# Kernel tuning notes

Hardware: AMD Instinct MI355X
Metric: run time of the kernel (lower is better)

Reference implementation:

```python
import jax, jax.numpy as jnp
import numpy as np

B, T, NN, H = 16, 64, 4096, 1024  # batch, seq_len, num_nodes**2, gru hidden


def _gru_layer(x, w_ih, w_hh, b_ih, b_hh):
    """PyTorch-semantics GRU layer, batch_first. x: [B, T, in] -> [B, T, H]."""
    h_dim = w_hh.shape[1]
    # precompute all input-side gate projections in one GEMM: [B, T, 3H]
    gates_x = jnp.einsum('bti,gi->btg', x, w_ih) + b_ih

    def step(h, gx):
        gh = h @ w_hh.T + b_hh                      # [B, 3H]
        xr, xz, xn = jnp.split(gx, 3, axis=-1)
        hr, hz, hn = jnp.split(gh, 3, axis=-1)
        r = jax.nn.sigmoid(xr + hr)
        z = jax.nn.sigmoid(xz + hz)
        n = jnp.tanh(xn + r * hn)
        h_new = (1.0 - z) * n + z * h
        return h_new, h_new

    h0 = jnp.zeros((x.shape[0], h_dim), x.dtype)
    _, ys = jax.lax.scan(step, h0, jnp.swapaxes(gates_x, 0, 1))  # time-major scan
    return jnp.swapaxes(ys, 0, 1)


def setup_inputs() -> dict:
    key = jax.random.key(0)
    ks = jax.random.split(key, 12)
    s_in, s_h = 1.0 / np.sqrt(NN), 1.0 / np.sqrt(H)
    return {
        'x':       jax.random.normal(ks[0], (B, T, NN), jnp.float32),
        'w_ih_l0': jax.random.normal(ks[1], (3 * H, NN), jnp.float32) * s_in,
        'w_hh_l0': jax.random.normal(ks[2], (3 * H, H), jnp.float32) * s_h,
        'b_ih_l0': jax.random.normal(ks[3], (3 * H,), jnp.float32) * s_h,
        'b_hh_l0': jax.random.normal(ks[4], (3 * H,), jnp.float32) * s_h,
        'w_ih_l1': jax.random.normal(ks[5], (3 * H, H), jnp.float32) * s_h,
        'w_hh_l1': jax.random.normal(ks[6], (3 * H, H), jnp.float32) * s_h,
        'b_ih_l1': jax.random.normal(ks[7], (3 * H,), jnp.float32) * s_h,
        'b_hh_l1': jax.random.normal(ks[8], (3 * H,), jnp.float32) * s_h,
        'dec_w':   jax.random.normal(ks[9], (NN, H), jnp.float32) * s_h,
        'dec_b':   jax.random.normal(ks[10], (NN,), jnp.float32) * s_h,
    }


def reference(x, w_ih_l0, w_hh_l0, b_ih_l0, b_hh_l0,
              w_ih_l1, w_hh_l1, b_ih_l1, b_hh_l1, dec_w, dec_b):
    # 2-layer GRU encode (batch_first), no dropout (eval / drop_p=0)
    h1 = _gru_layer(x, w_ih_l0, w_hh_l0, b_ih_l0, b_hh_l0)
    h2 = _gru_layer(h1, w_ih_l1, w_hh_l1, b_ih_l1, b_hh_l1)
    last = h2[:, -1, :]                               # [B, H] last timestep
    # per-sample decoder loop in the original == one batched GEMM here
    pred_graph_adj = last @ dec_w.T + dec_b           # [B, num_nodes**2]
    return pred_graph_adj
```

## Files before the change

### kernel.cpp

```cpp
#include <hip/hip_runtime.h>
#include <math.h>

constexpr int kB = 16;
constexpr int kT = 64;
constexpr int kH = 1024;

typedef short bf16x8 __attribute__((ext_vector_type(8)));
typedef float floatx4 __attribute__((ext_vector_type(4)));

__device__ __forceinline__ unsigned short f2bf_rne(float f) {
    unsigned u = __float_as_uint(f);
    u = u + 0x7FFFu + ((u >> 16) & 1u);
    return (unsigned short)(u >> 16);
}
__device__ __forceinline__ unsigned f2bf_fast_u(float f) {
    return (__float_as_uint(f) + 0x8000u) >> 16;
}
__device__ __forceinline__ uint4 pack8(const float4 a, const float4 b) {
    uint4 r;
    r.x = f2bf_fast_u(a.x) | (f2bf_fast_u(a.y) << 16);
    r.y = f2bf_fast_u(a.z) | (f2bf_fast_u(a.w) << 16);
    r.z = f2bf_fast_u(b.x) | (f2bf_fast_u(b.y) << 16);
    r.w = f2bf_fast_u(b.z) | (f2bf_fast_u(b.w) << 16);
    return r;
}

__device__ __forceinline__ void store_short_sys(unsigned short* p, unsigned v) {
    asm volatile("global_store_short %0, %1, off sc0 sc1"
                 :: "v"(p), "v"(v) : "memory");
}
__device__ __forceinline__ void store_dword_sys(unsigned* p, unsigned v) {
    asm volatile("global_store_dword %0, %1, off sc0 sc1"
                 :: "v"(p), "v"(v) : "memory");
}
__device__ __forceinline__ unsigned load_dword_sys(const unsigned* p) {
    unsigned v;
    asm volatile("global_load_dword %0, %1, off sc0 sc1\n\t"
                 "s_waitcnt vmcnt(0)"
                 : "=v"(v) : "v"(p) : "memory");
    return v;
}

__global__ __launch_bounds__(256)
void pack_bf16(const float* __restrict__ src, unsigned short* __restrict__ dst,
               int n4)
{
    const int i = blockIdx.x * 256 + threadIdx.x;
    if (i < n4) {
        const float4 v = ((const float4*)src)[i];
        ushort4 o;
        o.x = f2bf_rne(v.x); o.y = f2bf_rne(v.y);
        o.z = f2bf_rne(v.z); o.w = f2bf_rne(v.w);
        ((ushort4*)dst)[i] = o;
    }
}

#define GBM 64
#define GBN 64
#define GBK 16
#define GPAD 4

__global__ __launch_bounds__(256)
void gemm_nt_bias(const float* __restrict__ X, const float* __restrict__ W,
                  const float* __restrict__ bias, float* __restrict__ C,
                  int M, int N, int K)
{
    __shared__ float Xs[GBK][GBM + GPAD];
    __shared__ float Ws[GBK][GBN + GPAD];

    const int tid = threadIdx.x;
    const int bm = blockIdx.y * GBM;
    const int bn = blockIdx.x * GBN;
    const int tm = (tid >> 4) * 4;
    const int tn = (tid & 15) * 4;
    const int lr = tid >> 2;
    const int lc = (tid & 3) * 4;

    float acc[4][4] = {};

    for (int k0 = 0; k0 < K; k0 += GBK) {
        {
            const int gr = bm + lr;
            float4 v = make_float4(0.f, 0.f, 0.f, 0.f);
            if (gr < M) v = *(const float4*)(X + (long)gr * K + k0 + lc);
            Xs[lc + 0][lr] = v.x; Xs[lc + 1][lr] = v.y;
            Xs[lc + 2][lr] = v.z; Xs[lc + 3][lr] = v.w;
        }
        {
            const int gr = bn + lr;
            const float4 v = *(const float4*)(W + (long)gr * K + k0 + lc);
            Ws[lc + 0][lr] = v.x; Ws[lc + 1][lr] = v.y;
            Ws[lc + 2][lr] = v.z; Ws[lc + 3][lr] = v.w;
        }
        __syncthreads();
        #pragma unroll
        for (int k = 0; k < GBK; ++k) {
            const float4 a4 = *(const float4*)&Xs[k][tm];
            const float4 b4 = *(const float4*)&Ws[k][tn];
            acc[0][0] += a4.x * b4.x; acc[0][1] += a4.x * b4.y; acc[0][2] += a4.x * b4.z; acc[0][3] += a4.x * b4.w;
            acc[1][0] += a4.y * b4.x; acc[1][1] += a4.y * b4.y; acc[1][2] += a4.y * b4.z; acc[1][3] += a4.y * b4.w;
            acc[2][0] += a4.z * b4.x; acc[2][1] += a4.z * b4.y; acc[2][2] += a4.z * b4.z; acc[2][3] += a4.z * b4.w;
            acc[3][0] += a4.w * b4.x; acc[3][1] += a4.w * b4.y; acc[3][2] += a4.w * b4.z; acc[3][3] += a4.w * b4.w;
        }
        __syncthreads();
    }

    #pragma unroll
    for (int i = 0; i < 4; ++i) {
        const int gr = bm + tm + i;
        if (gr >= M) continue;
        #pragma unroll
        for (int jj = 0; jj < 4; ++jj) {
            const int gc = bn + tn + jj;
            C[(long)gr * N + gc] = acc[i][jj] + bias[gc];
        }
    }
}

__global__ __launch_bounds__(256)
void gemm_mfma_a(const float* __restrict__ X,
                 const float* __restrict__ W,
                 const float* __restrict__ bias,
                 float* __restrict__ C,
                 int M, int N, int K)
{
    __shared__ __attribute__((aligned(16))) unsigned short As[64 * 40];
    __shared__ __attribute__((aligned(16))) unsigned short Bs[128 * 40];

    const int tid  = threadIdx.x;
    const int lane = tid & 63;
    const int w    = tid >> 6;
    const int qm   = w & 1;
    const int qn   = w >> 1;
    const int bm   = blockIdx.y * 64;
    const int bn   = blockIdx.x * 128;
    const int al   = lane & 15;
    const int aq   = lane >> 4;

    floatx4 acc[2][4];
    #pragma unroll
    for (int i = 0; i < 2; ++i)
        #pragma unroll
        for (int j = 0; j < 4; ++j)
            acc[i][j] = (floatx4){0.f, 0.f, 0.f, 0.f};

    const int ar = tid >> 2;
    const int ak = (tid & 3) * 8;

    for (int k0 = 0; k0 < K; k0 += 32) {
        const float* ap = X + (long)(bm + ar) * K + k0 + ak;
        const float4 av0 = *(const float4*)(ap);
        const float4 av1 = *(const float4*)(ap + 4);
        float4 bv0[2], bv1[2];
        #pragma unroll
        for (int l = 0; l < 2; ++l) {
            const int c = tid + 256 * l;
            const float* bp = W + (long)(bn + (c >> 2)) * K + k0 + (c & 3) * 8;
            bv0[l] = *(const float4*)(bp);
            bv1[l] = *(const float4*)(bp + 4);
        }
        __syncthreads();
        *(uint4*)&As[ar * 40 + ak] = pack8(av0, av1);
        #pragma unroll
        for (int l = 0; l < 2; ++l) {
            const int c = tid + 256 * l;
            *(uint4*)&Bs[(c >> 2) * 40 + (c & 3) * 8] = pack8(bv0[l], bv1[l]);
        }
        __syncthreads();

        bf16x8 a[2], b[4];
        #pragma unroll
        for (int i = 0; i < 2; ++i)
            a[i] = *(const bf16x8*)&As[(qm * 32 + i * 16 + al) * 40 + aq * 8];
        #pragma unroll
        for (int j = 0; j < 4; ++j)
            b[j] = *(const bf16x8*)&Bs[(qn * 64 + j * 16 + al) * 40 + aq * 8];
        #pragma unroll
        for (int i = 0; i < 2; ++i)
            #pragma unroll
            for (int j = 0; j < 4; ++j)
                acc[i][j] = __builtin_amdgcn_mfma_f32_16x16x32_bf16(
                    a[i], b[j], acc[i][j], 0, 0, 0);
    }

    #pragma unroll
    for (int i = 0; i < 2; ++i) {
        #pragma unroll
        for (int j = 0; j < 4; ++j) {
            const int row0 = bm + qm * 32 + i * 16 + aq * 4;
            const int col  = bn + qn * 64 + j * 16 + al;
            const float bv = bias[col];
            #pragma unroll
            for (int r = 0; r < 4; ++r)
                C[(long)(row0 + r) * N + col] = acc[i][j][r] + bv;
        }
    }
}

#define FLAG_STRIDE 4

__global__ __launch_bounds__(768, 3)
void fused_gru_persistent(const float* __restrict__ gx0,
                          const unsigned short* __restrict__ w0, const float* __restrict__ bb0,
                          const unsigned short* __restrict__ w1, const float* __restrict__ bb1,
                          const unsigned short* __restrict__ w2, const float* __restrict__ bb2,
                          unsigned short* __restrict__ h1bf0, unsigned short* __restrict__ h1bf1,
                          unsigned short* __restrict__ h2bf0, unsigned short* __restrict__ h2bf1,
                          float* __restrict__ h2last, unsigned* __restrict__ flags)
{
    __shared__ __attribute__((aligned(16))) floatx4 part[12][3][64];

    const int tid   = threadIdx.x;
    const int lane  = tid & 63;
    const int wid   = tid >> 6;
    const int bx    = blockIdx.x;
    const int jbase = bx * 16;

    const int m  = wid >> 2;
    const int kh = wid & 3;
    const int al = lane & 15;
    const int aq = lane >> 4;

    const unsigned short* Wm = (m == 0) ? w0 : (m == 1) ? w1 : w2;
    const long wbase = (long)(jbase + al) * kH + kh * 256 + aq * 8;
    bf16x8 wreg[3][8];
    #pragma unroll
    for (int g = 0; g < 3; ++g)
        #pragma unroll
        for (int s = 0; s < 8; ++s)
            wreg[g][s] = *(const bf16x8*)(Wm + (long)g * kH * kH + wbase + s * 32);

    const int ub  = tid >> 4;
    const int ujj = tid & 15;
    const int ujg = jbase + ujj;
    const float b0r = bb0[ujg], b0z = bb0[kH + ujg], b0n = bb0[2 * kH + ujg];
    const float b1r = bb1[ujg], b1z = bb1[kH + ujg], b1n = bb1[2 * kH + ujg];
    const float b2r = bb2[ujg], b2z = bb2[kH + ujg], b2n = bb2[2 * kH + ujg];

    float h1reg = 0.f;
    float h2reg = 0.f;

    const int aoff = al * kH + kh * 256 + aq * 8;
    const int pl   = (ub >> 2) * 16 + ujj;
    const int pr   = ub & 3;

    float gxr = 0.f, gxz = 0.f, gxn = 0.f;
    if (tid < 256) {
        const float* g = gx0 + (long)ub * (kT * 3 * kH);
        gxr = g[ujg]; gxz = g[kH + ujg]; gxn = g[2 * kH + ujg];
    }

    for (int k = 0; k <= kT; ++k) {
        const unsigned short* h1p = (k & 1) ? h1bf0 : h1bf1;
        unsigned short*       h1o = (k & 1) ? h1bf1 : h1bf0;
        const unsigned short* h2p = (k & 1) ? h2bf1 : h2bf0;
        unsigned short*       h2o = (k & 1) ? h2bf0 : h2bf1;

        const bool azero = (m < 2) ? (k == 0) : (k <= 1);
        const unsigned short* hsrc = (m < 2) ? h1p : h2p;
        bf16x8 a[8];
        if (!azero) {
            #pragma unroll
            for (int s = 0; s < 8; ++s)
                asm volatile("global_load_dwordx4 %0, %1, off sc0 sc1"
                             : "=&v"(a[s]) : "v"(hsrc + aoff + s * 32) : "memory");
            asm volatile("s_waitcnt vmcnt(0)" ::: "memory");
            __builtin_amdgcn_sched_barrier(0);
        } else {
            #pragma unroll
            for (int s = 0; s < 8; ++s)
                a[s] = (bf16x8){0, 0, 0, 0, 0, 0, 0, 0};
        }

        floatx4 acc[3];
        #pragma unroll
        for (int g = 0; g < 3; ++g) acc[g] = (floatx4){0.f, 0.f, 0.f, 0.f};
        #pragma unroll
        for (int s = 0; s < 8; ++s)
            #pragma unroll
            for (int g = 0; g < 3; ++g)
                acc[g] = __builtin_amdgcn_mfma_f32_16x16x32_bf16(
                    a[s], wreg[g][s], acc[g], 0, 0, 0);

        #pragma unroll
        for (int g = 0; g < 3; ++g)
            part[wid][g][lane] = acc[g];
        __syncthreads();

        if (tid < 256) {
            float gh[3][3];
            #pragma unroll
            for (int mm = 0; mm < 3; ++mm)
                #pragma unroll
                for (int g = 0; g < 3; ++g)
                    gh[mm][g] = part[mm * 4 + 0][g][pl][pr] + part[mm * 4 + 1][g][pl][pr]
                              + part[mm * 4 + 2][g][pl][pr] + part[mm * 4 + 3][g][pl][pr];

            if (k < kT) {
                const float hr = gh[0][0] + b0r;
                const float hz = gh[0][1] + b0z;
                const float hn = gh[0][2] + b0n;
                const float r = 1.f / (1.f + __expf(-(gxr + hr)));
                const float z = 1.f / (1.f + __expf(-(gxz + hz)));
                const float n = tanhf(gxn + r * hn);
                const float hnew = (1.f - z) * n + z * h1reg;
                h1reg = hnew;
                store_short_sys(h1o + ub * kH + ujg, f2bf_fast_u(hnew));
            }
            if (k > 0) {
                const float xr = gh[1][0] + b1r;
                const float xz = gh[1][1] + b1z;
                const float xn = gh[1][2] + b1n;
                const float hr = gh[2][0] + b2r;
                const float hz = gh[2][1] + b2z;
                const float hn = gh[2][2] + b2n;
                const float r = 1.f / (1.f + __expf(-(xr + hr)));
                const float z = 1.f / (1.f + __expf(-(xz + hz)));
                const float n = tanhf(xn + r * hn);
                const float hnew = (1.f - z) * n + z * h2reg;
                h2reg = hnew;
                store_short_sys(h2o + ub * kH + ujg, f2bf_fast_u(hnew));
                if (k == kT) h2last[(long)ub * kH + ujg] = hnew;
            }
        }

        float nxr = 0.f, nxz = 0.f, nxn = 0.f;
        if (tid < 256 && (k + 1) < kT) {
            const float* g = gx0 + (long)ub * (kT * 3 * kH) + (long)(k + 1) * 3 * kH;
            nxr = g[ujg]; nxz = g[kH + ujg]; nxn = g[2 * kH + ujg];
        }

        if (k < kT) {
            __syncthreads();
            if (wid == 0) {
                const unsigned gen = (unsigned)(k + 1);
                if (lane == 0)
                    store_dword_sys(&flags[bx * FLAG_STRIDE], gen);
                while (load_dword_sys(&flags[lane * FLAG_STRIDE]) < gen) {}
            }
            __syncthreads();
        }

        gxr = nxr; gxz = nxz; gxn = nxn;
    }
}

extern "C" void kernel_launch(void* const* d_in, const int* in_sizes, int n_in,
                              void* d_out, int out_size, void* d_ws, size_t ws_size,
                              hipStream_t stream)
{
    const float* x        = (const float*)d_in[0];
    const float* w_ih_l0  = (const float*)d_in[1];
    const float* w_hh_l0  = (const float*)d_in[2];
    const float* b_ih_l0  = (const float*)d_in[3];
    const float* b_hh_l0  = (const float*)d_in[4];
    const float* w_ih_l1  = (const float*)d_in[5];
    const float* w_hh_l1  = (const float*)d_in[6];
    const float* b_ih_l1  = (const float*)d_in[7];
    const float* b_hh_l1  = (const float*)d_in[8];
    const float* dec_w    = (const float*)d_in[9];
    const float* dec_b    = (const float*)d_in[10];
    float* out = (float*)d_out;

    float* ws    = (float*)d_ws;
    float* gx0   = ws;
    unsigned short* h1bf0 = (unsigned short*)(gx0 + (size_t)1024 * 3072);
    unsigned short* h1bf1 = h1bf0 + (size_t)kB * kH;
    unsigned short* h2bf0 = h1bf1 + (size_t)kB * kH;
    unsigned short* h2bf1 = h2bf0 + (size_t)kB * kH;
    float* h2last = (float*)(h2bf1 + (size_t)kB * kH);
    unsigned short* wbf0 = (unsigned short*)(h2last + (size_t)kB * kH);
    unsigned short* wbf1 = wbf0 + (size_t)3 * kH * kH;
    unsigned short* wbf2 = wbf1 + (size_t)3 * kH * kH;
    unsigned* flags = (unsigned*)(wbf2 + (size_t)3 * kH * kH);

    (void)hipMemsetAsync(flags, 0, 64 * FLAG_STRIDE * sizeof(unsigned), stream);

    const int wn4 = 3 * kH * kH / 4;

    pack_bf16<<<(wn4 + 255) / 256, 256, 0, stream>>>(w_hh_l0, wbf0, wn4);
    pack_bf16<<<(wn4 + 255) / 256, 256, 0, stream>>>(w_ih_l1, wbf1, wn4);
    pack_bf16<<<(wn4 + 255) / 256, 256, 0, stream>>>(w_hh_l1, wbf2, wn4);

    gemm_mfma_a<<<dim3(3072 / 128, 1024 / 64), 256, 0, stream>>>(
        x, w_ih_l0, b_ih_l0, gx0, 1024, 3072, 4096);

    fused_gru_persistent<<<64, 768, 0, stream>>>(
        gx0, wbf0, b_hh_l0, wbf1, b_ih_l1, wbf2, b_hh_l1,
        h1bf0, h1bf1, h2bf0, h2bf1, h2last, flags);

    gemm_nt_bias<<<dim3(4096 / GBN, 1), 256, 0, stream>>>(
        h2last, dec_w, dec_b, out, kB, 4096, 1024);
}
```

Measured before the change: 691.9 us.

## Batch hidden-state stores via LDS staging and use a master-gated grid barrier

Each block now stages its new bf16 h1/h2 values in shared memory, and wave 0 writes them with a few system-coherent dwordx2 stores instead of per-thread 2-byte stores. The all-to-all flag polling is replaced by a centralized barrier: block 0 gathers the 64 flags and publishes a single go flag, and the other blocks spin on it with s_sleep. tanhf is replaced by a clamped exp-based tanh. The aim is to cut per-step barrier and store latency in the 64-step recurrence, at the cost of an extra hop through block 0 and slightly different tanh accuracy.

```diff
diff --git a/kernel.cpp b/kernel.cpp
--- a/kernel.cpp
+++ b/kernel.cpp
@@ -7,6 +7,7 @@
 
 typedef short bf16x8 __attribute__((ext_vector_type(8)));
 typedef float floatx4 __attribute__((ext_vector_type(4)));
+typedef unsigned uintx2 __attribute__((ext_vector_type(2)));
 
 __device__ __forceinline__ unsigned short f2bf_rne(float f) {
     unsigned u = __float_as_uint(f);
@@ -25,12 +26,18 @@
     return r;
 }
 
-__device__ __forceinline__ void store_short_sys(unsigned short* p, unsigned v) {
-    asm volatile("global_store_short %0, %1, off sc0 sc1"
-                 :: "v"(p), "v"(v) : "memory");
-}
+__device__ __forceinline__ float fast_tanh(float x) {
+    const float xc = fminf(fmaxf(x, -15.f), 15.f);
+    const float e = __expf(2.f * xc);
+    return (e - 1.f) / (e + 1.f);
+}
+
 __device__ __forceinline__ void store_dword_sys(unsigned* p, unsigned v) {
     asm volatile("global_store_dword %0, %1, off sc0 sc1"
+                 :: "v"(p), "v"(v) : "memory");
+}
+__device__ __forceinline__ void store_dwordx2_sys(void* p, uintx2 v) {
+    asm volatile("global_store_dwordx2 %0, %1, off sc0 sc1"
                  :: "v"(p), "v"(v) : "memory");
 }
 __device__ __forceinline__ unsigned load_dword_sys(const unsigned* p) {
@@ -209,6 +216,8 @@
                           float* __restrict__ h2last, unsigned* __restrict__ flags)
 {
     __shared__ __attribute__((aligned(16))) floatx4 part[12][3][64];
+    __shared__ __attribute__((aligned(16))) unsigned short h1stage[256];
+    __shared__ __attribute__((aligned(16))) unsigned short h2stage[256];
 
     const int tid   = threadIdx.x;
     const int lane  = tid & 63;
@@ -220,6 +229,8 @@
     const int kh = wid & 3;
     const int al = lane & 15;
     const int aq = lane >> 4;
+
+    unsigned* const go = flags + 64 * FLAG_STRIDE;
 
     const unsigned short* Wm = (m == 0) ? w0 : (m == 1) ? w1 : w2;
     const long wbase = (long)(jbase + al) * kH + kh * 256 + aq * 8;
@@ -244,6 +255,9 @@
     const int pl   = (ub >> 2) * 16 + ujj;
     const int pr   = ub & 3;
 
+    const int pb = lane >> 2;
+    const int pc = (lane & 3) * 4;
+
     float gxr = 0.f, gxz = 0.f, gxn = 0.f;
     if (tid < 256) {
         const float* g = gx0 + (long)ub * (kT * 3 * kH);
@@ -302,10 +316,10 @@
                 const float hn = gh[0][2] + b0n;
                 const float r = 1.f / (1.f + __expf(-(gxr + hr)));
                 const float z = 1.f / (1.f + __expf(-(gxz + hz)));
-                const float n = tanhf(gxn + r * hn);
+                const float n = fast_tanh(gxn + r * hn);
                 const float hnew = (1.f - z) * n + z * h1reg;
                 h1reg = hnew;
-                store_short_sys(h1o + ub * kH + ujg, f2bf_fast_u(hnew));
+                h1stage[tid] = (unsigned short)f2bf_fast_u(hnew);
             }
             if (k > 0) {
                 const float xr = gh[1][0] + b1r;
@@ -316,10 +330,10 @@
                 const float hn = gh[2][2] + b2n;
                 const float r = 1.f / (1.f + __expf(-(xr + hr)));
                 const float z = 1.f / (1.f + __expf(-(xz + hz)));
-                const float n = tanhf(xn + r * hn);
+                const float n = fast_tanh(xn + r * hn);
                 const float hnew = (1.f - z) * n + z * h2reg;
                 h2reg = hnew;
-                store_short_sys(h2o + ub * kH + ujg, f2bf_fast_u(hnew));
+                h2stage[tid] = (unsigned short)f2bf_fast_u(hnew);
                 if (k == kT) h2last[(long)ub * kH + ujg] = hnew;
             }
         }
@@ -333,10 +347,26 @@
         if (k < kT) {
             __syncthreads();
             if (wid == 0) {
+                {
+                    const uintx2 v = *(const uintx2*)&h1stage[pb * 16 + pc];
+                    store_dwordx2_sys(h1o + (long)pb * kH + jbase + pc, v);
+                }
+                if (k > 0) {
+                    const uintx2 v = *(const uintx2*)&h2stage[pb * 16 + pc];
+                    store_dwordx2_sys(h2o + (long)pb * kH + jbase + pc, v);
+                }
+                asm volatile("s_waitcnt vmcnt(0)" ::: "memory");
                 const unsigned gen = (unsigned)(k + 1);
                 if (lane == 0)
                     store_dword_sys(&flags[bx * FLAG_STRIDE], gen);
-                while (load_dword_sys(&flags[lane * FLAG_STRIDE]) < gen) {}
+                if (bx == 0) {
+                    while (load_dword_sys(&flags[lane * FLAG_STRIDE]) < gen)
+                        __builtin_amdgcn_s_sleep(1);
+                    if (lane == 0) store_dword_sys(go, gen);
+                } else {
+                    while (load_dword_sys(go) < gen)
+                        __builtin_amdgcn_s_sleep(1);
+                }
             }
             __syncthreads();
         }
@@ -374,7 +404,7 @@
     unsigned short* wbf2 = wbf1 + (size_t)3 * kH * kH;
     unsigned* flags = (unsigned*)(wbf2 + (size_t)3 * kH * kH);
 
-    (void)hipMemsetAsync(flags, 0, 64 * FLAG_STRIDE * sizeof(unsigned), stream);
+    (void)hipMemsetAsync(flags, 0, 4096, stream);
 
     const int wn4 = 3 * kH * kH / 4;
 
```

Measured after the change: 719.5 us. 1.04x slower.

## Pre-pack input GEMM operands to bf16 and use direct global-to-LDS loads

Applied to the files above, without the earlier changes.

Adds bf16 packing passes for x and w_ih_l0, then replaces the fp32-reading MFMA GEMM with a bf16 GEMM that loads tiles via global_load_lds into unpadded shared memory. The tile grows to 128x128 per block. This aims to cut the register-staged conversion and global traffic inside the GEMM, at the cost of extra pack kernels that write 32MB, more workspace, and possible LDS bank conflicts from removing padding.

```diff
diff --git a/kernel.cpp b/kernel.cpp
--- a/kernel.cpp
+++ b/kernel.cpp
@@ -15,14 +15,6 @@
 }
 __device__ __forceinline__ unsigned f2bf_fast_u(float f) {
     return (__float_as_uint(f) + 0x8000u) >> 16;
-}
-__device__ __forceinline__ uint4 pack8(const float4 a, const float4 b) {
-    uint4 r;
-    r.x = f2bf_fast_u(a.x) | (f2bf_fast_u(a.y) << 16);
-    r.y = f2bf_fast_u(a.z) | (f2bf_fast_u(a.w) << 16);
-    r.z = f2bf_fast_u(b.x) | (f2bf_fast_u(b.y) << 16);
-    r.w = f2bf_fast_u(b.z) | (f2bf_fast_u(b.w) << 16);
-    return r;
 }
 
 __device__ __forceinline__ void store_short_sys(unsigned short* p, unsigned v) {
@@ -39,6 +31,13 @@
                  "s_waitcnt vmcnt(0)"
                  : "=v"(v) : "v"(p) : "memory");
     return v;
+}
+
+__device__ __forceinline__ void gload_lds16(const unsigned short* g,
+                                            unsigned short* lds) {
+    __builtin_amdgcn_global_load_lds(
+        (const __attribute__((address_space(1))) unsigned int*)(g),
+        (__attribute__((address_space(3))) unsigned int*)(lds), 16, 0, 0);
 }
 
 __global__ __launch_bounds__(256)
@@ -118,77 +117,68 @@
 }
 
 __global__ __launch_bounds__(256)
-void gemm_mfma_a(const float* __restrict__ X,
-                 const float* __restrict__ W,
+void gemm_bf16_a(const unsigned short* __restrict__ X,
+                 const unsigned short* __restrict__ W,
                  const float* __restrict__ bias,
                  float* __restrict__ C,
                  int M, int N, int K)
 {
-    __shared__ __attribute__((aligned(16))) unsigned short As[64 * 40];
-    __shared__ __attribute__((aligned(16))) unsigned short Bs[128 * 40];
+    __shared__ __attribute__((aligned(16))) unsigned short As[128 * 32];
+    __shared__ __attribute__((aligned(16))) unsigned short Bs[128 * 32];
 
     const int tid  = threadIdx.x;
     const int lane = tid & 63;
     const int w    = tid >> 6;
-    const int qm   = w & 1;
-    const int qn   = w >> 1;
-    const int bm   = blockIdx.y * 64;
+    const int wm   = w & 1;
+    const int wn   = w >> 1;
+    const int bm   = blockIdx.y * 128;
     const int bn   = blockIdx.x * 128;
     const int al   = lane & 15;
     const int aq   = lane >> 4;
 
-    floatx4 acc[2][4];
+    const int srow = lane >> 2;
+    const int scol = (lane & 3) * 8;
+
+    floatx4 acc[4][4];
     #pragma unroll
-    for (int i = 0; i < 2; ++i)
+    for (int i = 0; i < 4; ++i)
         #pragma unroll
         for (int j = 0; j < 4; ++j)
             acc[i][j] = (floatx4){0.f, 0.f, 0.f, 0.f};
 
-    const int ar = tid >> 2;
-    const int ak = (tid & 3) * 8;
-
     for (int k0 = 0; k0 < K; k0 += 32) {
-        const float* ap = X + (long)(bm + ar) * K + k0 + ak;
-        const float4 av0 = *(const float4*)(ap);
-        const float4 av1 = *(const float4*)(ap + 4);
-        float4 bv0[2], bv1[2];
-        #pragma unroll
-        for (int l = 0; l < 2; ++l) {
-            const int c = tid + 256 * l;
-            const float* bp = W + (long)(bn + (c >> 2)) * K + k0 + (c & 3) * 8;
-            bv0[l] = *(const float4*)(bp);
-            bv1[l] = *(const float4*)(bp + 4);
-        }
-        __syncthreads();
-        *(uint4*)&As[ar * 40 + ak] = pack8(av0, av1);
-        #pragma unroll
-        for (int l = 0; l < 2; ++l) {
-            const int c = tid + 256 * l;
-            *(uint4*)&Bs[(c >> 2) * 40 + (c & 3) * 8] = pack8(bv0[l], bv1[l]);
-        }
-        __syncthreads();
-
-        bf16x8 a[2], b[4];
-        #pragma unroll
-        for (int i = 0; i < 2; ++i)
-            a[i] = *(const bf16x8*)&As[(qm * 32 + i * 16 + al) * 40 + aq * 8];
+        #pragma unroll
+        for (int i = 0; i < 2; ++i) {
+            const int r = (w * 2 + i) * 16 + srow;
+            gload_lds16(X + (size_t)(bm + r) * K + k0 + scol,
+                        As + (w * 2 + i) * 512);
+            gload_lds16(W + (size_t)(bn + r) * K + k0 + scol,
+                        Bs + (w * 2 + i) * 512);
+        }
+        __syncthreads();
+
+        bf16x8 af[4], bf[4];
+        #pragma unroll
+        for (int i = 0; i < 4; ++i)
+            af[i] = *(const bf16x8*)&As[(wm * 64 + i * 16 + al) * 32 + aq * 8];
         #pragma unroll
         for (int j = 0; j < 4; ++j)
-            b[j] = *(const bf16x8*)&Bs[(qn * 64 + j * 16 + al) * 40 + aq * 8];
-        #pragma unroll
-        for (int i = 0; i < 2; ++i)
+            bf[j] = *(const bf16x8*)&Bs[(wn * 64 + j * 16 + al) * 32 + aq * 8];
+        #pragma unroll
+        for (int i = 0; i < 4; ++i)
             #pragma unroll
             for (int j = 0; j < 4; ++j)
                 acc[i][j] = __builtin_amdgcn_mfma_f32_16x16x32_bf16(
-                    a[i], b[j], acc[i][j], 0, 0, 0);
+                    af[i], bf[j], acc[i][j], 0, 0, 0);
+        __syncthreads();
     }
 
     #pragma unroll
-    for (int i = 0; i < 2; ++i) {
+    for (int i = 0; i < 4; ++i) {
         #pragma unroll
         for (int j = 0; j < 4; ++j) {
-            const int row0 = bm + qm * 32 + i * 16 + aq * 4;
-            const int col  = bn + qn * 64 + j * 16 + al;
+            const int row0 = bm + wm * 64 + i * 16 + aq * 4;
+            const int col  = bn + wn * 64 + j * 16 + al;
             const float bv = bias[col];
             #pragma unroll
             for (int r = 0; r < 4; ++r)
@@ -372,18 +362,24 @@
     unsigned short* wbf0 = (unsigned short*)(h2last + (size_t)kB * kH);
     unsigned short* wbf1 = wbf0 + (size_t)3 * kH * kH;
     unsigned short* wbf2 = wbf1 + (size_t)3 * kH * kH;
-    unsigned* flags = (unsigned*)(wbf2 + (size_t)3 * kH * kH);
-
-    (void)hipMemsetAsync(flags, 0, 64 * FLAG_STRIDE * sizeof(unsigned), stream);
+    unsigned short* xbf  = wbf2 + (size_t)3 * kH * kH;
+    unsigned short* wihbf = xbf + (size_t)1024 * 4096;
+    unsigned* flags = (unsigned*)(wihbf + (size_t)3072 * 4096);
+
+    (void)hipMemsetAsync(flags, 0, 4096, stream);
 
     const int wn4 = 3 * kH * kH / 4;
+    const int xn4 = 1024 * 4096 / 4;
+    const int win4 = 3072 * 4096 / 4;
 
     pack_bf16<<<(wn4 + 255) / 256, 256, 0, stream>>>(w_hh_l0, wbf0, wn4);
     pack_bf16<<<(wn4 + 255) / 256, 256, 0, stream>>>(w_ih_l1, wbf1, wn4);
     pack_bf16<<<(wn4 + 255) / 256, 256, 0, stream>>>(w_hh_l1, wbf2, wn4);
-
-    gemm_mfma_a<<<dim3(3072 / 128, 1024 / 64), 256, 0, stream>>>(
-        x, w_ih_l0, b_ih_l0, gx0, 1024, 3072, 4096);
+    pack_bf16<<<(xn4 + 255) / 256, 256, 0, stream>>>(x, xbf, xn4);
+    pack_bf16<<<(win4 + 255) / 256, 256, 0, stream>>>(w_ih_l0, wihbf, win4);
+
+    gemm_bf16_a<<<dim3(3072 / 128, 1024 / 128), 256, 0, stream>>>(
+        xbf, wihbf, b_ih_l0, gx0, 1024, 3072, 4096);
 
     fused_gru_persistent<<<64, 768, 0, stream>>>(
         gx0, wbf0, b_hh_l0, wbf1, b_ih_l1, wbf2, b_hh_l1,
```

Result: faster. 670.4 us (-3.1%).
